# Kernel tuning notes

Measured on AMD Instinct MI355X. Metric: run time of the kernel, lower is better.

Reference implementation:

```python
import jax, jax.numpy as jnp
import numpy as np

VOCAB, E, H, L, B, T = 32000, 64, 8, 25, 1000, 512


def setup_inputs() -> dict:
    key = jax.random.key(0)
    ks = jax.random.split(key, 6)
    return {
        "x": jax.random.randint(ks[0], (B, T), 0, VOCAB),
        "h_0": jnp.zeros((L, B, H), jnp.float32),
        "embedding": jax.random.normal(ks[1], (VOCAB, E), jnp.float32) * 0.02,
        "W_xh0": jax.random.normal(ks[2], (E, H), jnp.float32) / np.float32(np.sqrt(E)),
        "W_xh_rest": jax.random.normal(ks[3], (L - 1, H, H), jnp.float32) / np.float32(np.sqrt(H)),
        "W_hh": jax.random.normal(ks[4], (L, H, H), jnp.float32) / np.float32(np.sqrt(H)),
        "b_h": jnp.zeros((L, H), jnp.float32),
        "W_hy": jax.random.normal(ks[5], (H, 1), jnp.float32) / np.float32(np.sqrt(H)),
        "b_y": jnp.zeros((1,), jnp.float32),
    }


def reference(x, h_0, embedding, W_xh0, W_xh_rest, W_hh, b_h, W_hy, b_y):
    # x: [B, T] int ids; embedded: [B, T, E]
    emb = embedding[x]
    n_layers = h_0.shape[0]

    def step(h, e_t):  # h: [L, B, H], e_t: [B, E]
        inp = e_t
        hs = []
        for i in range(n_layers):  # fixed small layer count -> unrolled
            W = W_xh0 if i == 0 else W_xh_rest[i - 1]
            h_i = jnp.tanh(inp @ W + h[i] @ W_hh[i] + b_h[i])
            hs.append(h_i)
            inp = h_i
        return jnp.stack(hs, 0), None

    h_last, _ = jax.lax.scan(step, h_0, jnp.swapaxes(emb, 0, 1))  # scan over time
    logits = h_last[-1] @ W_hy + b_y  # [B, 1]
    return logits.squeeze(1), h_last
```

## Files before the change

### kernel.cpp

```cpp
#include <hip/hip_runtime.h>

#define VOCAB 32000
#define E 64
#define H 8
#define L 25
#define B 1000
#define T 512

#define CHUNK 8
#define NCHUNK (T / CHUNK)
#define NSTEP (NCHUNK + L - 1)
#define THREADS 256

#define LAYER_STRIDE 132
#define LDS_FLOATS (L * LAYER_STRIDE)

typedef float v2f __attribute__((ext_vector_type(2)));

__global__ __launch_bounds__(256) void proj_kernel(
    const float* __restrict__ emb, const float* __restrict__ w0,
    float* __restrict__ ptab)
{
    __shared__ float w0s[E * H];
    int tid = threadIdx.x;
    w0s[tid] = w0[tid];
    w0s[tid + 256] = w0[tid + 256];
    __syncthreads();

    int r = blockIdx.x * 256 + tid;
    if (r >= VOCAB) return;
    const float4* e4 = (const float4*)(emb + r * E);
    const v2f* w2 = (const v2f*)w0s;
    v2f a0 = {0.f, 0.f}, a1 = {0.f, 0.f}, a2 = {0.f, 0.f}, a3 = {0.f, 0.f};
#pragma unroll
    for (int k4 = 0; k4 < E / 4; ++k4) {
        float4 v = e4[k4];
        int kb = k4 * 16;
        a0 += (v2f){v.x, v.x} * w2[kb + 0];  a1 += (v2f){v.x, v.x} * w2[kb + 1];
        a2 += (v2f){v.x, v.x} * w2[kb + 2];  a3 += (v2f){v.x, v.x} * w2[kb + 3];
        a0 += (v2f){v.y, v.y} * w2[kb + 4];  a1 += (v2f){v.y, v.y} * w2[kb + 5];
        a2 += (v2f){v.y, v.y} * w2[kb + 6];  a3 += (v2f){v.y, v.y} * w2[kb + 7];
        a0 += (v2f){v.z, v.z} * w2[kb + 8];  a1 += (v2f){v.z, v.z} * w2[kb + 9];
        a2 += (v2f){v.z, v.z} * w2[kb + 10]; a3 += (v2f){v.z, v.z} * w2[kb + 11];
        a0 += (v2f){v.w, v.w} * w2[kb + 12]; a1 += (v2f){v.w, v.w} * w2[kb + 13];
        a2 += (v2f){v.w, v.w} * w2[kb + 14]; a3 += (v2f){v.w, v.w} * w2[kb + 15];
    }
    float4* o4 = (float4*)(ptab + r * 8);
    o4[0] = (float4){a0.x, a0.y, a1.x, a1.y};
    o4[1] = (float4){a2.x, a2.y, a3.x, a3.y};
}

__device__ __forceinline__ float fast_tanh(float x) {
    float t = __builtin_amdgcn_exp2f(x * 2.8853900817779268f);
    float r = __builtin_amdgcn_rcpf(1.0f + t);
    return __builtin_fmaf(-2.0f, r, 1.0f);
}

__device__ __forceinline__ float dpp_xor1(float x) {
    return __int_as_float(__builtin_amdgcn_mov_dpp(__float_as_int(x), 0xB1, 0xF, 0xF, true));
}
__device__ __forceinline__ float dpp_xor2(float x) {
    return __int_as_float(__builtin_amdgcn_mov_dpp(__float_as_int(x), 0x4E, 0xF, 0xF, true));
}
__device__ __forceinline__ float dpp_xor8(float x) {
    return __int_as_float(__builtin_amdgcn_mov_dpp(__float_as_int(x), 0x128, 0xF, 0xF, true));
}

__global__ __launch_bounds__(THREADS) void rnn_recur(
    const int*   __restrict__ x,
    const float* __restrict__ h0,
    const float* __restrict__ wrest,
    const float* __restrict__ whh_g,
    const float* __restrict__ bh,
    const float* __restrict__ why,
    const float* __restrict__ by,
    const float* __restrict__ ptab,
    float*       __restrict__ out)
{
    __shared__ __align__(16) float buf[LDS_FLOATS];

    const int tid = threadIdx.x;
    const int row = tid >> 4;
    const int lp  = tid & 15;
    const int j   = (lp & 3) | ((lp >> 3) << 2);
    const int g   = row * 2 + ((lp >> 2) & 1);
    const bool active = g < L;
    const int gc  = active ? g : 0;
    const int b = blockIdx.x;

    v2f wh01 = {0.f, 0.f}, wh23 = {0.f, 0.f}, wh45 = {0.f, 0.f}, wh67 = {0.f, 0.f};
    v2f wx01 = {0.f, 0.f}, wx23 = {0.f, 0.f}, wx45 = {0.f, 0.f}, wx67 = {0.f, 0.f};
    v2f h01  = {0.f, 0.f}, h23  = {0.f, 0.f}, h45  = {0.f, 0.f}, h67  = {0.f, 0.f};
    float bias = 0.f;

    float* mybuf = &buf[gc * LAYER_STRIDE];
    const float* prevbuf = (gc > 0) ? (mybuf - LAYER_STRIDE) : mybuf;

    if (active) {
        const float* whL = whh_g + g * 64;
        wh01 = (v2f){whL[(j ^ 0) * 8 + j], whL[(j ^ 1) * 8 + j]};
        wh23 = (v2f){whL[(j ^ 2) * 8 + j], whL[(j ^ 3) * 8 + j]};
        wh45 = (v2f){whL[(j ^ 4) * 8 + j], whL[(j ^ 5) * 8 + j]};
        wh67 = (v2f){whL[(j ^ 6) * 8 + j], whL[(j ^ 7) * 8 + j]};
        if (g > 0) {
            const float* wxL = wrest + (g - 1) * 64;
            wx01 = (v2f){wxL[0 * 8 + j], wxL[1 * 8 + j]};
            wx23 = (v2f){wxL[2 * 8 + j], wxL[3 * 8 + j]};
            wx45 = (v2f){wxL[4 * 8 + j], wxL[5 * 8 + j]};
            wx67 = (v2f){wxL[6 * 8 + j], wxL[7 * 8 + j]};
        }
        bias = bh[g * 8 + j];
        const float* h0p = h0 + (g * B + b) * H;
        h01 = (v2f){h0p[j ^ 0], h0p[j ^ 1]};
        h23 = (v2f){h0p[j ^ 2], h0p[j ^ 3]};
        h45 = (v2f){h0p[j ^ 4], h0p[j ^ 5]};
        h67 = (v2f){h0p[j ^ 6], h0p[j ^ 7]};
    }

    const int xbase = b * T;
    float pv[CHUNK];
    if (active && g == 0) {
#pragma unroll
        for (int ct = 0; ct < CHUNK; ++ct)
            pv[ct] = ptab[x[xbase + ct] * H + j];
    }

    for (int s = 0; s < NSTEP; ++s) {
        const int c = s - g;
        if (active && (unsigned)c < (unsigned)NCHUNK) {
            const int p = c & 1;
            float* wptr = mybuf + p * (CHUNK * 8);
            const float4* ip4 = (const float4*)(prevbuf + p * (CHUNK * 8));

            int4 t0, t1;
            const bool pf = (g == 0) && (c + 1 < NCHUNK);
            if (pf) {
                const int4* xp4 = (const int4*)(x + xbase + (c + 1) * CHUNK);
                t0 = xp4[0];
                t1 = xp4[1];
            }

#pragma unroll
            for (int ct = 0; ct < CHUNK; ++ct) {
                v2f acc, acc2;
                if (g == 0) {
                    acc  = (v2f){pv[ct] + bias, 0.f};
                    acc2 = (v2f){0.f, 0.f};
                } else {
                    float4 ia = ip4[2 * ct];
                    float4 ib = ip4[2 * ct + 1];
                    acc   = (v2f){bias, 0.f};
                    acc  += (v2f){ia.x, ia.y} * wx01;
                    acc2  = (v2f){ia.z, ia.w} * wx23;
                    acc  += (v2f){ib.x, ib.y} * wx45;
                    acc2 += (v2f){ib.z, ib.w} * wx67;
                }
                acc  += h01 * wh01;
                acc2 += h23 * wh23;
                acc  += h45 * wh45;
                acc2 += h67 * wh67;
                v2f at = acc + acc2;
                float hn = fast_tanh(at.x + at.y);

                if (g < L - 1) wptr[ct * 8 + j] = hn;

                float o1 = dpp_xor1(hn);
                float q0 = dpp_xor2(hn);
                float q1 = dpp_xor2(o1);
                h01 = (v2f){hn, o1};
                h23 = (v2f){q0, q1};
                h45 = (v2f){dpp_xor8(hn), dpp_xor8(o1)};
                h67 = (v2f){dpp_xor8(q0), dpp_xor8(q1)};
            }

            if (pf) {
                pv[0] = ptab[t0.x * H + j];
                pv[1] = ptab[t0.y * H + j];
                pv[2] = ptab[t0.z * H + j];
                pv[3] = ptab[t0.w * H + j];
                pv[4] = ptab[t1.x * H + j];
                pv[5] = ptab[t1.y * H + j];
                pv[6] = ptab[t1.z * H + j];
                pv[7] = ptab[t1.w * H + j];
            }

            if (c == NCHUNK - 1) {
                out[B + (g * B + b) * H + j] = h01.x;
                if (g == L - 1) {
                    float lg = by[0];
                    lg += h01.x * why[j]     + h01.y * why[j ^ 1];
                    lg += h23.x * why[j ^ 2] + h23.y * why[j ^ 3];
                    lg += h45.x * why[j ^ 4] + h45.y * why[j ^ 5];
                    lg += h67.x * why[j ^ 6] + h67.y * why[j ^ 7];
                    if (j == 0) out[b] = lg;
                }
            }
        }
        __syncthreads();
    }
}

extern "C" void kernel_launch(void* const* d_in, const int* in_sizes, int n_in,
                              void* d_out, int out_size, void* d_ws, size_t ws_size,
                              hipStream_t stream) {
    const int*   x     = (const int*)d_in[0];
    const float* h0    = (const float*)d_in[1];
    const float* emb   = (const float*)d_in[2];
    const float* w0    = (const float*)d_in[3];
    const float* wrest = (const float*)d_in[4];
    const float* whh   = (const float*)d_in[5];
    const float* bh    = (const float*)d_in[6];
    const float* why   = (const float*)d_in[7];
    const float* by    = (const float*)d_in[8];
    float* out  = (float*)d_out;
    float* ptab = (float*)d_ws;

    hipLaunchKernelGGL(proj_kernel, dim3((VOCAB + 255) / 256), dim3(256),
                       0, stream, emb, w0, ptab);
    hipLaunchKernelGGL(rnn_recur, dim3(B), dim3(THREADS),
                       0, stream, x, h0, wrest, whh, bh, why, by, ptab, out);
}
```

Before: 242.4 us.

## Process two batch rows per block to interleave independent recurrence chains

Each block now handles two batch elements, keeping two sets of hidden-state registers and two LDS regions, and halves the grid size. The two independent dependency chains are interleaved to hide the latency of DPP, tanh and LDS traffic within the serial time recurrence, and they share weight registers and barriers. In exchange, per-thread register and LDS use roughly double and there are fewer blocks to spread across CUs, which can reduce occupancy.

```diff
diff --git a/kernel.cpp b/kernel.cpp
--- a/kernel.cpp
+++ b/kernel.cpp
@@ -13,7 +13,8 @@
 #define THREADS 256
 
 #define LAYER_STRIDE 132
-#define LDS_FLOATS (L * LAYER_STRIDE)
+#define BATCH_FLOATS (L * LAYER_STRIDE)
+#define LDS_FLOATS (2 * BATCH_FLOATS)
 
 typedef float v2f __attribute__((ext_vector_type(2)));
 
@@ -86,15 +87,19 @@
     const int g   = row * 2 + ((lp >> 2) & 1);
     const bool active = g < L;
     const int gc  = active ? g : 0;
-    const int b = blockIdx.x;
+    const int b0 = blockIdx.x * 2;
+    const int b1 = b0 + 1;
 
     v2f wh01 = {0.f, 0.f}, wh23 = {0.f, 0.f}, wh45 = {0.f, 0.f}, wh67 = {0.f, 0.f};
     v2f wx01 = {0.f, 0.f}, wx23 = {0.f, 0.f}, wx45 = {0.f, 0.f}, wx67 = {0.f, 0.f};
-    v2f h01  = {0.f, 0.f}, h23  = {0.f, 0.f}, h45  = {0.f, 0.f}, h67  = {0.f, 0.f};
+    v2f hA01 = {0.f, 0.f}, hA23 = {0.f, 0.f}, hA45 = {0.f, 0.f}, hA67 = {0.f, 0.f};
+    v2f hB01 = {0.f, 0.f}, hB23 = {0.f, 0.f}, hB45 = {0.f, 0.f}, hB67 = {0.f, 0.f};
     float bias = 0.f;
 
-    float* mybuf = &buf[gc * LAYER_STRIDE];
-    const float* prevbuf = (gc > 0) ? (mybuf - LAYER_STRIDE) : mybuf;
+    float* mybufA = &buf[gc * LAYER_STRIDE];
+    float* mybufB = mybufA + BATCH_FLOATS;
+    const float* prevbufA = (gc > 0) ? (mybufA - LAYER_STRIDE) : mybufA;
+    const float* prevbufB = prevbufA + BATCH_FLOATS;
 
     if (active) {
         const float* whL = whh_g + g * 64;
@@ -110,89 +115,141 @@
             wx67 = (v2f){wxL[6 * 8 + j], wxL[7 * 8 + j]};
         }
         bias = bh[g * 8 + j];
-        const float* h0p = h0 + (g * B + b) * H;
-        h01 = (v2f){h0p[j ^ 0], h0p[j ^ 1]};
-        h23 = (v2f){h0p[j ^ 2], h0p[j ^ 3]};
-        h45 = (v2f){h0p[j ^ 4], h0p[j ^ 5]};
-        h67 = (v2f){h0p[j ^ 6], h0p[j ^ 7]};
-    }
-
-    const int xbase = b * T;
-    float pv[CHUNK];
+        const float* hA0p = h0 + (g * B + b0) * H;
+        const float* hB0p = h0 + (g * B + b1) * H;
+        hA01 = (v2f){hA0p[j ^ 0], hA0p[j ^ 1]};
+        hA23 = (v2f){hA0p[j ^ 2], hA0p[j ^ 3]};
+        hA45 = (v2f){hA0p[j ^ 4], hA0p[j ^ 5]};
+        hA67 = (v2f){hA0p[j ^ 6], hA0p[j ^ 7]};
+        hB01 = (v2f){hB0p[j ^ 0], hB0p[j ^ 1]};
+        hB23 = (v2f){hB0p[j ^ 2], hB0p[j ^ 3]};
+        hB45 = (v2f){hB0p[j ^ 4], hB0p[j ^ 5]};
+        hB67 = (v2f){hB0p[j ^ 6], hB0p[j ^ 7]};
+    }
+
+    const int xbaseA = b0 * T;
+    const int xbaseB = b1 * T;
+    float pvA[CHUNK], pvB[CHUNK];
     if (active && g == 0) {
 #pragma unroll
-        for (int ct = 0; ct < CHUNK; ++ct)
-            pv[ct] = ptab[x[xbase + ct] * H + j];
+        for (int ct = 0; ct < CHUNK; ++ct) {
+            pvA[ct] = ptab[x[xbaseA + ct] * H + j];
+            pvB[ct] = ptab[x[xbaseB + ct] * H + j];
+        }
     }
 
     for (int s = 0; s < NSTEP; ++s) {
         const int c = s - g;
         if (active && (unsigned)c < (unsigned)NCHUNK) {
             const int p = c & 1;
-            float* wptr = mybuf + p * (CHUNK * 8);
-            const float4* ip4 = (const float4*)(prevbuf + p * (CHUNK * 8));
-
-            int4 t0, t1;
+            float* wptrA = mybufA + p * (CHUNK * 8);
+            float* wptrB = mybufB + p * (CHUNK * 8);
+            const float4* ip4A = (const float4*)(prevbufA + p * (CHUNK * 8));
+            const float4* ip4B = (const float4*)(prevbufB + p * (CHUNK * 8));
+
+            int4 tA0, tA1, tB0, tB1;
             const bool pf = (g == 0) && (c + 1 < NCHUNK);
             if (pf) {
-                const int4* xp4 = (const int4*)(x + xbase + (c + 1) * CHUNK);
-                t0 = xp4[0];
-                t1 = xp4[1];
+                const int4* xpA = (const int4*)(x + xbaseA + (c + 1) * CHUNK);
+                const int4* xpB = (const int4*)(x + xbaseB + (c + 1) * CHUNK);
+                tA0 = xpA[0]; tA1 = xpA[1];
+                tB0 = xpB[0]; tB1 = xpB[1];
             }
 
 #pragma unroll
             for (int ct = 0; ct < CHUNK; ++ct) {
-                v2f acc, acc2;
+                v2f accA, accA2, accB, accB2;
                 if (g == 0) {
-                    acc  = (v2f){pv[ct] + bias, 0.f};
-                    acc2 = (v2f){0.f, 0.f};
+                    accA  = (v2f){pvA[ct] + bias, 0.f};
+                    accA2 = (v2f){0.f, 0.f};
+                    accB  = (v2f){pvB[ct] + bias, 0.f};
+                    accB2 = (v2f){0.f, 0.f};
                 } else {
-                    float4 ia = ip4[2 * ct];
-                    float4 ib = ip4[2 * ct + 1];
-                    acc   = (v2f){bias, 0.f};
-                    acc  += (v2f){ia.x, ia.y} * wx01;
-                    acc2  = (v2f){ia.z, ia.w} * wx23;
-                    acc  += (v2f){ib.x, ib.y} * wx45;
-                    acc2 += (v2f){ib.z, ib.w} * wx67;
+                    float4 iaA = ip4A[2 * ct];
+                    float4 ibA = ip4A[2 * ct + 1];
+                    float4 iaB = ip4B[2 * ct];
+                    float4 ibB = ip4B[2 * ct + 1];
+                    accA   = (v2f){bias, 0.f};
+                    accA  += (v2f){iaA.x, iaA.y} * wx01;
+                    accA2  = (v2f){iaA.z, iaA.w} * wx23;
+                    accA  += (v2f){ibA.x, ibA.y} * wx45;
+                    accA2 += (v2f){ibA.z, ibA.w} * wx67;
+                    accB   = (v2f){bias, 0.f};
+                    accB  += (v2f){iaB.x, iaB.y} * wx01;
+                    accB2  = (v2f){iaB.z, iaB.w} * wx23;
+                    accB  += (v2f){ibB.x, ibB.y} * wx45;
+                    accB2 += (v2f){ibB.z, ibB.w} * wx67;
                 }
-                acc  += h01 * wh01;
-                acc2 += h23 * wh23;
-                acc  += h45 * wh45;
-                acc2 += h67 * wh67;
-                v2f at = acc + acc2;
-                float hn = fast_tanh(at.x + at.y);
-
-                if (g < L - 1) wptr[ct * 8 + j] = hn;
-
-                float o1 = dpp_xor1(hn);
-                float q0 = dpp_xor2(hn);
-                float q1 = dpp_xor2(o1);
-                h01 = (v2f){hn, o1};
-                h23 = (v2f){q0, q1};
-                h45 = (v2f){dpp_xor8(hn), dpp_xor8(o1)};
-                h67 = (v2f){dpp_xor8(q0), dpp_xor8(q1)};
+                accA  += hA01 * wh01;
+                accA2 += hA23 * wh23;
+                accA  += hA45 * wh45;
+                accA2 += hA67 * wh67;
+                accB  += hB01 * wh01;
+                accB2 += hB23 * wh23;
+                accB  += hB45 * wh45;
+                accB2 += hB67 * wh67;
+                v2f atA = accA + accA2;
+                v2f atB = accB + accB2;
+                float hnA = fast_tanh(atA.x + atA.y);
+                float hnB = fast_tanh(atB.x + atB.y);
+
+                if (g < L - 1) {
+                    wptrA[ct * 8 + j] = hnA;
+                    wptrB[ct * 8 + j] = hnB;
+                }
+
+                float oA1 = dpp_xor1(hnA);
+                float oB1 = dpp_xor1(hnB);
+                float qA0 = dpp_xor2(hnA);
+                float qB0 = dpp_xor2(hnB);
+                float qA1 = dpp_xor2(oA1);
+                float qB1 = dpp_xor2(oB1);
+                hA01 = (v2f){hnA, oA1};
+                hB01 = (v2f){hnB, oB1};
+                hA23 = (v2f){qA0, qA1};
+                hB23 = (v2f){qB0, qB1};
+                hA45 = (v2f){dpp_xor8(hnA), dpp_xor8(oA1)};
+                hB45 = (v2f){dpp_xor8(hnB), dpp_xor8(oB1)};
+                hA67 = (v2f){dpp_xor8(qA0), dpp_xor8(qA1)};
+                hB67 = (v2f){dpp_xor8(qB0), dpp_xor8(qB1)};
             }
 
             if (pf) {
-                pv[0] = ptab[t0.x * H + j];
-                pv[1] = ptab[t0.y * H + j];
-                pv[2] = ptab[t0.z * H + j];
-                pv[3] = ptab[t0.w * H + j];
-                pv[4] = ptab[t1.x * H + j];
-                pv[5] = ptab[t1.y * H + j];
-                pv[6] = ptab[t1.z * H + j];
-                pv[7] = ptab[t1.w * H + j];
+                pvA[0] = ptab[tA0.x * H + j];
+                pvA[1] = ptab[tA0.y * H + j];
+                pvA[2] = ptab[tA0.z * H + j];
+                pvA[3] = ptab[tA0.w * H + j];
+                pvA[4] = ptab[tA1.x * H + j];
+                pvA[5] = ptab[tA1.y * H + j];
+                pvA[6] = ptab[tA1.z * H + j];
+                pvA[7] = ptab[tA1.w * H + j];
+                pvB[0] = ptab[tB0.x * H + j];
+                pvB[1] = ptab[tB0.y * H + j];
+                pvB[2] = ptab[tB0.z * H + j];
+                pvB[3] = ptab[tB0.w * H + j];
+                pvB[4] = ptab[tB1.x * H + j];
+                pvB[5] = ptab[tB1.y * H + j];
+                pvB[6] = ptab[tB1.z * H + j];
+                pvB[7] = ptab[tB1.w * H + j];
             }
 
             if (c == NCHUNK - 1) {
-                out[B + (g * B + b) * H + j] = h01.x;
+                out[B + (g * B + b0) * H + j] = hA01.x;
+                out[B + (g * B + b1) * H + j] = hB01.x;
                 if (g == L - 1) {
-                    float lg = by[0];
-                    lg += h01.x * why[j]     + h01.y * why[j ^ 1];
-                    lg += h23.x * why[j ^ 2] + h23.y * why[j ^ 3];
-                    lg += h45.x * why[j ^ 4] + h45.y * why[j ^ 5];
-                    lg += h67.x * why[j ^ 6] + h67.y * why[j ^ 7];
-                    if (j == 0) out[b] = lg;
+                    float lgA = by[0], lgB = by[0];
+                    lgA += hA01.x * why[j]     + hA01.y * why[j ^ 1];
+                    lgB += hB01.x * why[j]     + hB01.y * why[j ^ 1];
+                    lgA += hA23.x * why[j ^ 2] + hA23.y * why[j ^ 3];
+                    lgB += hB23.x * why[j ^ 2] + hB23.y * why[j ^ 3];
+                    lgA += hA45.x * why[j ^ 4] + hA45.y * why[j ^ 5];
+                    lgB += hB45.x * why[j ^ 4] + hB45.y * why[j ^ 5];
+                    lgA += hA67.x * why[j ^ 6] + hA67.y * why[j ^ 7];
+                    lgB += hB67.x * why[j ^ 6] + hB67.y * why[j ^ 7];
+                    if (j == 0) {
+                        out[b0] = lgA;
+                        out[b1] = lgB;
+                    }
                 }
             }
         }
@@ -217,6 +274,6 @@
 
     hipLaunchKernelGGL(proj_kernel, dim3((VOCAB + 255) / 256), dim3(256),
                        0, stream, emb, w0, ptab);
-    hipLaunchKernelGGL(rnn_recur, dim3(B), dim3(THREADS),
+    hipLaunchKernelGGL(rnn_recur, dim3(B / 2), dim3(THREADS),
                        0, stream, x, h0, wrest, whh, bh, why, by, ptab, out);
 }
```

Measured after the change: 269.3 us. 11.1% more time.
